# Performance work log

Hardware: AMD Instinct MI355X
Metric: run time of the kernel (lower is better)

Reference implementation:

```python
import jax, jax.numpy as jnp
import numpy as np

DIM = 64
B_GRAPHS = 16
N_NODES = 4096
N_EDGES = 16384
SLOPE = 0.01  # PyTorch leaky_relu default negative slope


def lrelu(x):
    return jnp.where(x >= 0, x, SLOPE * x)


def setup_inputs() -> dict:
    key = jax.random.key(0)
    ks = jax.random.split(key, 16)
    d = DIM

    def rn(k, shape, scale=0.05):
        return jax.random.normal(k, shape, dtype=jnp.float32) * scale

    def z(*s):
        return jnp.zeros(s, jnp.float32)

    return {
        "x": jax.random.normal(ks[0], (N_NODES, 3), dtype=jnp.float32),
        "edge_attr": jax.random.normal(ks[1], (N_EDGES, 4), dtype=jnp.float32),
        "edge_index": jax.random.randint(ks[2], (2, N_EDGES), 0, N_NODES),
        "batch": jnp.sort(jax.random.randint(ks[3], (N_NODES,), 0, B_GRAPHS)),
        # lin0
        "W0": rn(ks[4], (3, d)), "b0": z(d),
        # edge MLP: Linear(4,d) -> LeakyReLU -> Linear(d, d*d)
        "We1": rn(ks[5], (4, d)), "be1": z(d),
        "We2": rn(ks[6], (d, d * d), 0.01), "be2": z(d * d),
        # NNConv root weight + bias
        "root": rn(ks[7], (d, d)), "conv_b": z(d),
        # GRU(d, d)  (PyTorch layout: [3d, in] / [3d, hid], gate order r,z,n)
        "Wih": rn(ks[8], (3 * d, d)), "Whh": rn(ks[9], (3 * d, d)),
        "bih": z(3 * d), "bhh": z(3 * d),
        # Set2Set LSTM(2d, d)  (gate order i,f,g,o)
        "lWih": rn(ks[10], (4 * d, 2 * d)), "lWhh": rn(ks[11], (4 * d, d)),
        "lbih": z(4 * d), "lbhh": z(4 * d),
        # lin_out: Linear(2d, 2)
        "Wout": rn(ks[12], (2 * d, 2)), "bout": z(2),
    }


def _forward(x, edge_attr, W0, b0, We1, be1, We2, be2, root, conv_b,
             Wih, Whh, bih, bhh, lWih, lWhh, lbih, lbhh, Wout, bout,
             edge_index, batch):
    d = DIM
    N = x.shape[0]
    E = edge_attr.shape[0]
    src, dst = edge_index[0], edge_index[1]  # messages flow src(j) -> dst(i)

    out = lrelu(x @ W0 + b0)  # [N, d]
    h = out                    # GRU hidden state (h = out.unsqueeze(0))

    # Edge-conditioned weights: constant across the 6 iterations, compute once.
    he = lrelu(edge_attr @ We1 + be1)          # [E, d]
    W_e = (he @ We2 + be2).reshape(E, d, d)    # [E, d, d]
    deg = jax.ops.segment_sum(jnp.ones((E,), jnp.float32), dst, num_segments=N)
    inv_deg = (1.0 / jnp.maximum(deg, 1.0))[:, None]  # mean aggr, clamp like PyG

    for _ in range(6):
        # NNConv: gather x_j, per-edge matmul, scatter-mean, plus root term
        msg = jnp.einsum('ed,edf->ef', out[src], W_e)            # [E, d]
        agg = jax.ops.segment_sum(msg, dst, num_segments=N) * inv_deg
        m = lrelu(agg + out @ root + conv_b)                     # [N, d]
        # GRU cell (single step, PyTorch gate order r, z, n)
        gi = m @ Wih.T + bih
        gh = h @ Whh.T + bhh
        i_r, i_z, i_n = jnp.split(gi, 3, axis=-1)
        h_r, h_z, h_n = jnp.split(gh, 3, axis=-1)
        r = jax.nn.sigmoid(i_r + h_r)
        zg = jax.nn.sigmoid(i_z + h_z)
        n = jnp.tanh(i_n + r * h_n)
        h = (1.0 - zg) * n + zg * h
        out = h

    # Set2Set pooling, processing_steps = 1
    Bg = B_GRAPHS
    q_star = jnp.zeros((Bg, 2 * d), jnp.float32)
    hl = jnp.zeros((Bg, d), jnp.float32)
    cl = jnp.zeros((Bg, d), jnp.float32)
    gates = q_star @ lWih.T + lbih + hl @ lWhh.T + lbhh
    gi_, gf_, gg_, go_ = jnp.split(gates, 4, axis=-1)
    cl = jax.nn.sigmoid(gf_) * cl + jax.nn.sigmoid(gi_) * jnp.tanh(gg_)
    q = jax.nn.sigmoid(go_) * jnp.tanh(cl)         # [Bg, d]
    e = jnp.sum(out * q[batch], axis=-1)           # [N]
    emax = jax.ops.segment_max(e, batch, num_segments=Bg)
    a = jnp.exp(e - emax[batch])
    asum = jax.ops.segment_sum(a, batch, num_segments=Bg)
    a = a / asum[batch]                            # per-graph softmax attention
    rpool = jax.ops.segment_sum(a[:, None] * out, batch, num_segments=Bg)
    q_star = jnp.concatenate([q, rpool], axis=-1)  # [Bg, 2d]

    return q_star @ Wout + bout                    # [Bg, 2]


def reference(x, edge_attr, edge_index, batch, W0, b0, We1, be1, We2, be2,
              root, conv_b, Wih, Whh, bih, bhh, lWih, lWhh, lbih, lbhh,
              Wout, bout):
    return _forward(x, edge_attr, W0, b0, We1, be1, We2, be2, root, conv_b,
                    Wih, Whh, bih, bhh, lWih, lWhh, lbih, lbhh, Wout, bout,
                    edge_index, batch)
```

## Files before the change

kernel.cpp:

```cpp
#include <hip/hip_runtime.h>
#include <cstddef>

#define NE 16384
#define NN 4096
#define BG 16
#define CSTR 4416

__device__ __forceinline__ float lrelu(float v){ return v >= 0.f ? v : 0.01f*v; }
__device__ __forceinline__ float sigm(float v){ return 1.f/(1.f + expf(-v)); }

__global__ __launch_bounds__(256) void setup_kernel(
    const float* __restrict__ x, const float* __restrict__ ea,
    const int* __restrict__ ei,
    const float* __restrict__ W0, const float* __restrict__ b0,
    const float* __restrict__ We1, const float* __restrict__ be1,
    const float* __restrict__ We2, const float* __restrict__ be2,
    const float* __restrict__ root, const float* __restrict__ Whh,
    const float* __restrict__ Wih,
    float* __restrict__ Baug, float* __restrict__ WihT,
    float* __restrict__ h, float* __restrict__ he,
    int* __restrict__ deg, int* __restrict__ cnt)
{
    int t = blockIdx.x*256 + threadIdx.x;
    {
        int e = t >> 6, f = t & 63;
        float v = be1[f];
        #pragma unroll
        for (int d = 0; d < 4; ++d) v += ea[e*4+d]*We1[d*64+f];
        he[t] = lrelu(v);
    }
    if (t < 64*CSTR) {
        int d = t / CSTR, c = t - d*CSTR;
        float v;
        if (c < 4096)      v = We2[(c>>6)*4096 + d*64 + (c&63)];
        else if (c < 4160) v = be2[d*64 + (c-4096)];
        else if (c < 4352) v = Whh[(c-4160)*64 + d];
        else               v = root[d*64 + (c-4352)];
        Baug[t] = v;
    }
    if (t < NN*64) {
        int n = t >> 6, f = t & 63;
        float v = b0[f];
        #pragma unroll
        for (int d = 0; d < 3; ++d) v += x[n*3+d]*W0[d*64+f];
        h[t] = lrelu(v);
    }
    if (t < 12288) { int k = t / 192; WihT[t] = Wih[(t - k*192)*64 + k]; }
    if (t < NE) {
        atomicAdd(&deg[ei[NE + t]], 1);
        atomicAdd(&cnt[ei[t]], 1);
    }
}

__global__ __launch_bounds__(256) void scan_kernel(const int* __restrict__ cnt,
                                                   int* __restrict__ offs)
{
    __shared__ int ps[256];
    int t = threadIdx.x;
    int base = t*16;
    int loc[16];
    int s = 0;
    #pragma unroll
    for (int i = 0; i < 16; ++i) { loc[i] = s; s += cnt[base+i]; }
    ps[t] = s; __syncthreads();
    for (int off = 1; off < 256; off <<= 1) {
        int v = 0;
        if (t >= off) v = ps[t-off];
        __syncthreads();
        if (t >= off) ps[t] += v;
        __syncthreads();
    }
    int pre = (t == 0) ? 0 : ps[t-1];
    #pragma unroll
    for (int i = 0; i < 16; ++i) offs[base+i] = pre + loc[i];
    if (t == 255) offs[NN] = pre + s;
}

__global__ __launch_bounds__(256) void scatter_kernel(
    const int* __restrict__ ei, const int* __restrict__ offs,
    int* __restrict__ cnt,
    int* __restrict__ srcs, int* __restrict__ dsts, int* __restrict__ perm)
{
    int e = blockIdx.x*256 + threadIdx.x;
    if (e >= NE) return;
    int s = ei[e], d = ei[NE + e];
    int old = atomicSub(&cnt[s], 1);
    int pos = offs[s] + old - 1;
    srcs[pos] = s; dsts[pos] = d; perm[pos] = e;
}

__global__ __launch_bounds__(256) void inv_range_kernel(
    const int* __restrict__ deg, const int* __restrict__ batch,
    float* __restrict__ inv_deg, int* __restrict__ gstart, int* __restrict__ gend)
{
    int n = blockIdx.x*256 + threadIdx.x;
    if (n >= NN) return;
    inv_deg[n] = 1.f / fmaxf((float)deg[n], 1.f);
    int b  = batch[n];
    int bp = (n == 0)    ? -1 : batch[n-1];
    int bn = (n == NN-1) ? BG : batch[n+1];
    for (int g = bp+1; g <= b; ++g) gstart[g] = n;
    for (int g = b;   g <  bn; ++g) gend[g]   = n+1;
    if (n == 0)    for (int g = 0;   g < b;  ++g) gend[g]   = 0;
    if (n == NN-1) for (int g = b+1; g < BG; ++g) gstart[g] = NN;
}

__global__ __launch_bounds__(256) void gemm_big(
    const float* __restrict__ h, const float* __restrict__ Baug,
    float* __restrict__ C, float* __restrict__ agg)
{
    __shared__ float As[64][132];
    int t = threadIdx.x;
    int bx = blockIdx.x;
    int by = blockIdx.y;
    int m0 = by*128, c0 = bx*128;

    if (bx == 0) {
        float* a = agg + by*8192;
        #pragma unroll
        for (int i = 0; i < 32; ++i) a[t + i*256] = 0.f;
    }
    #pragma unroll
    for (int i = 0; i < 8; ++i) {
        int idx4 = t + i*256;
        int r = idx4 >> 4;
        int kc = (idx4 & 15) * 4;
        const float4 v = *(const float4*)(h + (size_t)(m0 + r)*64 + kc);
        As[kc+0][r] = v.x; As[kc+1][r] = v.y; As[kc+2][r] = v.z; As[kc+3][r] = v.w;
    }
    __syncthreads();

    int tx = t & 15, ty = t >> 4;
    int c_lo = c0 + tx*4, c_hi = c0 + 64 + tx*4;
    bool hi_ok = (c0 + 64) < CSTR;

    float acc[8][8];
    #pragma unroll
    for (int i = 0; i < 8; ++i)
        #pragma unroll
        for (int j = 0; j < 8; ++j) acc[i][j] = 0.f;

    #pragma unroll 8
    for (int k = 0; k < 64; ++k) {
        float4 a0 = *(const float4*)&As[k][ty*4];
        float4 a1 = *(const float4*)&As[k][64 + ty*4];
        float4 b0 = *(const float4*)(Baug + (size_t)k*CSTR + c_lo);
        float4 b1 = hi_ok ? *(const float4*)(Baug + (size_t)k*CSTR + c_hi)
                          : make_float4(0.f,0.f,0.f,0.f);
        float av[8] = {a0.x,a0.y,a0.z,a0.w,a1.x,a1.y,a1.z,a1.w};
        float bv[8] = {b0.x,b0.y,b0.z,b0.w,b1.x,b1.y,b1.z,b1.w};
        #pragma unroll
        for (int i = 0; i < 8; ++i)
            #pragma unroll
            for (int j = 0; j < 8; ++j) acc[i][j] += av[i]*bv[j];
    }

    #pragma unroll
    for (int i = 0; i < 8; ++i) {
        int m = m0 + (i>>2)*64 + ty*4 + (i&3);
        float* Cr = C + (size_t)m*CSTR;
        *(float4*)(Cr + c_lo) = make_float4(acc[i][0],acc[i][1],acc[i][2],acc[i][3]);
        if (hi_ok)
            *(float4*)(Cr + c_hi) = make_float4(acc[i][4],acc[i][5],acc[i][6],acc[i][7]);
    }
}

__global__ __launch_bounds__(256) void edge_kernel(
    const float* __restrict__ C, const float* __restrict__ he,
    const int* __restrict__ srcs, const int* __restrict__ dsts,
    const int* __restrict__ perm, float* __restrict__ agg)
{
    __shared__ float hs[256];
    int t = threadIdx.x;
    int e0 = blockIdx.x*4;
    int w = t >> 6, f = t & 63;
    int es = e0 + w;
    int pe = perm[es];
    hs[t] = he[(size_t)pe*64 + f];
    int src = srcs[es], dst = dsts[es];
    __syncthreads();
    const float* Cs = C + (size_t)src*CSTR;
    float m = Cs[4096 + f];
    #pragma unroll 8
    for (int k = 0; k < 64; ++k) m += hs[w*64+k] * Cs[k*64 + f];
    atomicAdd(&agg[(size_t)dst*64 + f], m);
}

__global__ __launch_bounds__(256) void node_kernel(
    const float* __restrict__ C, const float* __restrict__ agg,
    const float* __restrict__ inv_deg, const float* __restrict__ conv_b,
    const float* __restrict__ WihT, const float* __restrict__ bih,
    const float* __restrict__ bhh, float* __restrict__ h)
{
    __shared__ float WT[64][196];
    __shared__ float mT[64][18];
    int t = threadIdx.x;
    int n0 = blockIdx.x * 16;
    #pragma unroll
    for (int i = 0; i < 48; ++i) {
        int idx = t + i*256;
        int k = idx / 192;
        WT[k][idx - k*192] = WihT[idx];
    }
    #pragma unroll
    for (int i = 0; i < 4; ++i) {
        int idx = t + i*256;
        int n = idx >> 6, d = idx & 63;
        int gn = n0 + n;
        float v = agg[(size_t)gn*64 + d]*inv_deg[gn]
                + C[(size_t)gn*CSTR + 4352 + d] + conv_b[d];
        mT[d][n] = lrelu(v);
    }
    __syncthreads();

    int tx = t & 31, ty = t >> 5;
    float acc[2][2][3] = {};
    for (int k = 0; k < 64; ++k) {
        float2 a  = *(float2*)&mT[k][ty*2];
        float2 br = *(float2*)&WT[k][tx*2];
        float2 bz = *(float2*)&WT[k][64 + tx*2];
        float2 bn = *(float2*)&WT[k][128 + tx*2];
        acc[0][0][0] += a.x*br.x; acc[0][1][0] += a.x*br.y;
        acc[1][0][0] += a.y*br.x; acc[1][1][0] += a.y*br.y;
        acc[0][0][1] += a.x*bz.x; acc[0][1][1] += a.x*bz.y;
        acc[1][0][1] += a.y*bz.x; acc[1][1][1] += a.y*bz.y;
        acc[0][0][2] += a.x*bn.x; acc[0][1][2] += a.x*bn.y;
        acc[1][0][2] += a.y*bn.x; acc[1][1][2] += a.y*bn.y;
    }
    #pragma unroll
    for (int i = 0; i < 2; ++i) {
        int n = n0 + ty*2 + i;
        const float* Cn = C + (size_t)n*CSTR;
        #pragma unroll
        for (int j = 0; j < 2; ++j) {
            int g = tx*2 + j;
            float ir  = acc[i][j][0] + bih[g];
            float iz  = acc[i][j][1] + bih[64+g];
            float in_ = acc[i][j][2] + bih[128+g];
            float r  = sigm(ir  + Cn[4160 + g]       + bhh[g]);
            float z  = sigm(iz  + Cn[4160 + 64 + g]  + bhh[64+g]);
            float nn = tanhf(in_ + r*(Cn[4160 + 128 + g] + bhh[128+g]));
            float ho = h[(size_t)n*64 + g];
            h[(size_t)n*64 + g] = (1.f - z)*nn + z*ho;
        }
    }
}

__device__ __forceinline__ float q_val(const float* lbih, const float* lbhh, int g)
{
    float gi = lbih[g]     + lbhh[g];
    float gg = lbih[128+g] + lbhh[128+g];
    float go = lbih[192+g] + lbhh[192+g];
    return sigm(go)*tanhf(sigm(gi)*tanhf(gg));
}

__global__ __launch_bounds__(256) void e_kernel(
    const float* __restrict__ h, const float* __restrict__ lbih,
    const float* __restrict__ lbhh, float* __restrict__ e)
{
    __shared__ float qs[64];
    int t = threadIdx.x;
    if (t < 64) qs[t] = q_val(lbih, lbhh, t);
    __syncthreads();
    int w = t >> 6, f = t & 63;
    int n = blockIdx.x*4 + w;
    float p = h[(size_t)n*64 + f]*qs[f];
    #pragma unroll
    for (int off = 32; off; off >>= 1) p += __shfl_xor(p, off);
    if (f == 0) e[n] = p;
}

__global__ __launch_bounds__(1024) void pool_kernel(
    const float* __restrict__ h, float* __restrict__ e,
    const int* __restrict__ gstart, const int* __restrict__ gend,
    const float* __restrict__ lbih, const float* __restrict__ lbhh,
    const float* __restrict__ Wout, const float* __restrict__ bout,
    float* __restrict__ out)
{
    __shared__ float red[1024];
    __shared__ float rp[64];
    __shared__ float sval;
    int g = blockIdx.x, t = threadIdx.x;
    int s = gstart[g], en = gend[g];

    float mx = -1e30f;
    for (int n = s+t; n < en; n += 1024) mx = fmaxf(mx, e[n]);
    red[t] = mx; __syncthreads();
    for (int st = 512; st; st >>= 1) { if (t < st) red[t] = fmaxf(red[t], red[t+st]); __syncthreads(); }
    if (t == 0) sval = red[0];
    __syncthreads();
    float lmx = sval;
    __syncthreads();

    float sm = 0.f;
    for (int n = s+t; n < en; n += 1024) { float a = expf(e[n]-lmx); e[n] = a; sm += a; }
    red[t] = sm; __syncthreads();
    for (int st = 512; st; st >>= 1) { if (t < st) red[t] += red[t+st]; __syncthreads(); }
    if (t == 0) sval = (red[0] > 0.f) ? 1.f/red[0] : 0.f;
    __syncthreads();
    float inv_asum = sval;
    __syncthreads();

    int w = t >> 6, f = t & 63;
    float racc = 0.f;
    for (int n = s+w; n < en; n += 16) racc += e[n]*h[(size_t)n*64 + f];
    red[t] = racc; __syncthreads();
    if (w == 0) {
        float a = 0.f;
        #pragma unroll
        for (int i = 0; i < 16; ++i) a += red[i*64 + f];
        rp[f] = a*inv_asum;
    }
    __syncthreads();

    if (t < 64) {
        float qv = q_val(lbih, lbhh, t);
        float p0 = qv*Wout[t*2]   + rp[t]*Wout[(64+t)*2];
        float p1 = qv*Wout[t*2+1] + rp[t]*Wout[(64+t)*2+1];
        #pragma unroll
        for (int off = 32; off; off >>= 1) { p0 += __shfl_xor(p0, off); p1 += __shfl_xor(p1, off); }
        if (t == 0) { out[g*2] = p0 + bout[0]; out[g*2+1] = p1 + bout[1]; }
    }
}

extern "C" void kernel_launch(void* const* d_in, const int* in_sizes, int n_in,
                              void* d_out, int out_size, void* d_ws, size_t ws_size,
                              hipStream_t stream)
{
    const float* x      = (const float*)d_in[0];
    const float* ea     = (const float*)d_in[1];
    const int*   ei     = (const int*)  d_in[2];
    const int*   batch  = (const int*)  d_in[3];
    const float* W0     = (const float*)d_in[4];
    const float* b0     = (const float*)d_in[5];
    const float* We1    = (const float*)d_in[6];
    const float* be1    = (const float*)d_in[7];
    const float* We2    = (const float*)d_in[8];
    const float* be2    = (const float*)d_in[9];
    const float* root   = (const float*)d_in[10];
    const float* conv_b = (const float*)d_in[11];
    const float* Wih    = (const float*)d_in[12];
    const float* Whh    = (const float*)d_in[13];
    const float* bih    = (const float*)d_in[14];
    const float* bhh    = (const float*)d_in[15];
    const float* lbih   = (const float*)d_in[18];
    const float* lbhh   = (const float*)d_in[19];
    const float* Wout   = (const float*)d_in[20];
    const float* bout   = (const float*)d_in[21];
    float* out = (float*)d_out;

    float* W = (float*)d_ws;
    size_t off = 0;
    float* C       = W + off; off += (size_t)NN*CSTR;
    float* Baug    = W + off; off += (size_t)64*CSTR;
    float* h       = W + off; off += (size_t)NN*64;
    float* he      = W + off; off += (size_t)NE*64;
    float* agg     = W + off; off += (size_t)NN*64;
    float* WihT    = W + off; off += 12288;
    float* inv_deg = W + off; off += NN;
    float* e       = W + off; off += NN;
    int*   deg     = (int*)(W + off); off += NN;
    int*   cnt     = (int*)(W + off); off += NN;
    int*   offs    = (int*)(W + off); off += NN+1;
    int*   srcs    = (int*)(W + off); off += NE;
    int*   dsts    = (int*)(W + off); off += NE;
    int*   perm    = (int*)(W + off); off += NE;
    int*   gstart  = (int*)(W + off); off += BG;
    int*   gend    = (int*)(W + off); off += BG;

    hipMemsetAsync(deg, 0, 2*NN*sizeof(int), stream);
    setup_kernel<<<4096, 256, 0, stream>>>(x, ea, ei, W0, b0, We1, be1, We2, be2,
                                           root, Whh, Wih, Baug, WihT, h, he, deg, cnt);
    scan_kernel<<<1, 256, 0, stream>>>(cnt, offs);
    scatter_kernel<<<64, 256, 0, stream>>>(ei, offs, cnt, srcs, dsts, perm);
    inv_range_kernel<<<16, 256, 0, stream>>>(deg, batch, inv_deg, gstart, gend);

    for (int it = 0; it < 6; ++it) {
        gemm_big<<<dim3(35, 32), 256, 0, stream>>>(h, Baug, C, agg);
        edge_kernel<<<NE/4, 256, 0, stream>>>(C, he, srcs, dsts, perm, agg);
        node_kernel<<<NN/16, 256, 0, stream>>>(C, agg, inv_deg, conv_b, WihT, bih, bhh, h);
    }

    e_kernel<<<NN/4, 256, 0, stream>>>(h, lbih, lbhh, e);
    pool_kernel<<<BG, 1024, 0, stream>>>(h, e, gstart, gend, lbih, lbhh, Wout, bout, out);
}
```

Measured before the change: 658.3 us.

## Fuse per-node weight GEMM with edge messages in one conv kernel, drop C buffer

```diff
diff --git a/kernel.cpp b/kernel.cpp
--- a/kernel.cpp
+++ b/kernel.cpp
@@ -4,7 +4,8 @@
 #define NE 16384
 #define NN 4096
 #define BG 16
-#define CSTR 4416
+#define NT 16
+#define ACH 16
 
 __device__ __forceinline__ float lrelu(float v){ return v >= 0.f ? v : 0.01f*v; }
 __device__ __forceinline__ float sigm(float v){ return 1.f/(1.f + expf(-v)); }
@@ -14,10 +15,8 @@
     const int* __restrict__ ei,
     const float* __restrict__ W0, const float* __restrict__ b0,
     const float* __restrict__ We1, const float* __restrict__ be1,
-    const float* __restrict__ We2, const float* __restrict__ be2,
-    const float* __restrict__ root, const float* __restrict__ Whh,
-    const float* __restrict__ Wih,
-    float* __restrict__ Baug, float* __restrict__ WihT,
+    const float* __restrict__ Wih, const float* __restrict__ Whh,
+    float* __restrict__ WihT, float* __restrict__ WhhT,
     float* __restrict__ h, float* __restrict__ he,
     int* __restrict__ deg, int* __restrict__ cnt)
 {
@@ -29,15 +28,6 @@
         for (int d = 0; d < 4; ++d) v += ea[e*4+d]*We1[d*64+f];
         he[t] = lrelu(v);
     }
-    if (t < 64*CSTR) {
-        int d = t / CSTR, c = t - d*CSTR;
-        float v;
-        if (c < 4096)      v = We2[(c>>6)*4096 + d*64 + (c&63)];
-        else if (c < 4160) v = be2[d*64 + (c-4096)];
-        else if (c < 4352) v = Whh[(c-4160)*64 + d];
-        else               v = root[d*64 + (c-4352)];
-        Baug[t] = v;
-    }
     if (t < NN*64) {
         int n = t >> 6, f = t & 63;
         float v = b0[f];
@@ -45,7 +35,11 @@
         for (int d = 0; d < 3; ++d) v += x[n*3+d]*W0[d*64+f];
         h[t] = lrelu(v);
     }
-    if (t < 12288) { int k = t / 192; WihT[t] = Wih[(t - k*192)*64 + k]; }
+    if (t < 12288) {
+        int k = t / 192, g = t - k*192;
+        WihT[t] = Wih[g*64 + k];
+        WhhT[t] = Whh[g*64 + k];
+    }
     if (t < NE) {
         atomicAdd(&deg[ei[NE + t]], 1);
         atomicAdd(&cnt[ei[t]], 1);
@@ -87,6 +81,14 @@
     int old = atomicSub(&cnt[s], 1);
     int pos = offs[s] + old - 1;
     srcs[pos] = s; dsts[pos] = d; perm[pos] = e;
+}
+
+__global__ __launch_bounds__(256) void reorder_kernel(
+    const float* __restrict__ he, const int* __restrict__ perm,
+    float* __restrict__ he_srt)
+{
+    int t = blockIdx.x*256 + threadIdx.x;
+    he_srt[t] = he[(size_t)perm[t>>6]*64 + (t & 63)];
 }
 
 __global__ __launch_bounds__(256) void inv_range_kernel(
@@ -105,143 +107,185 @@
     if (n == NN-1) for (int g = b+1; g < BG; ++g) gstart[g] = NN;
 }
 
-__global__ __launch_bounds__(256) void gemm_big(
-    const float* __restrict__ h, const float* __restrict__ Baug,
-    float* __restrict__ C, float* __restrict__ agg)
-{
-    __shared__ float As[64][132];
-    int t = threadIdx.x;
-    int bx = blockIdx.x;
-    int by = blockIdx.y;
-    int m0 = by*128, c0 = bx*128;
-
-    if (bx == 0) {
-        float* a = agg + by*8192;
-        #pragma unroll
-        for (int i = 0; i < 32; ++i) a[t + i*256] = 0.f;
-    }
-    #pragma unroll
-    for (int i = 0; i < 8; ++i) {
-        int idx4 = t + i*256;
-        int r = idx4 >> 4;
-        int kc = (idx4 & 15) * 4;
-        const float4 v = *(const float4*)(h + (size_t)(m0 + r)*64 + kc);
-        As[kc+0][r] = v.x; As[kc+1][r] = v.y; As[kc+2][r] = v.z; As[kc+3][r] = v.w;
-    }
-    __syncthreads();
-
-    int tx = t & 15, ty = t >> 4;
-    int c_lo = c0 + tx*4, c_hi = c0 + 64 + tx*4;
-    bool hi_ok = (c0 + 64) < CSTR;
-
-    float acc[8][8];
-    #pragma unroll
-    for (int i = 0; i < 8; ++i)
-        #pragma unroll
-        for (int j = 0; j < 8; ++j) acc[i][j] = 0.f;
-
+__global__ __launch_bounds__(1024) void conv_kernel(
+    const float* __restrict__ h, const float* __restrict__ We2,
+    const float* __restrict__ be2, const float* __restrict__ he_srt,
+    const int* __restrict__ offs, const int* __restrict__ srcs,
+    const int* __restrict__ dsts, float* __restrict__ agg)
+{
+    __shared__ float hsT[64][NT];
+    __shared__ float Tb [NT][64];
+    __shared__ float Tc [ACH][NT][64];
+    int t  = threadIdx.x;
+    int n0 = blockIdx.x * NT;
+
+    {
+        int n = t >> 6, i = t & 63;
+        hsT[i][n] = h[(size_t)(n0+n)*64 + i];
+    }
+    __syncthreads();
+    {
+        int n = t >> 6, f = t & 63;
+        float acc = 0.f;
+        #pragma unroll 8
+        for (int i = 0; i < 64; ++i) acc += hsT[i][n] * be2[i*64+f];
+        Tb[n][f] = acc;
+    }
+
+    int ebase = offs[n0];
+    int ecnt  = offs[n0+NT] - ebase;
+    int eend  = ebase + ecnt;
+    int slot  = t >> 4;
+    int f4    = (t & 15) * 4;
+    int e0 = ebase + slot, e1 = ebase + slot + 64;
+    int nl0 = -1, dt0 = 0, nl1 = -1, dt1 = 0;
+    if (slot < ecnt)       { nl0 = srcs[e0] - n0; dt0 = dsts[e0]; }
+    if (slot + 64 < ecnt)  { nl1 = srcs[e1] - n0; dt1 = dsts[e1]; }
+    float4 m0 = {0,0,0,0}, m1 = {0,0,0,0};
+
+    int aT = t >> 6;
+    int fT = (t & 15) * 4;
+    int nT = ((t >> 4) & 3) * 4;
+
+    for (int c = 0; c < 4; ++c) {
+        const float* Wp = We2 + ((size_t)(c*ACH + aT))*4096 + fT;
+        float4 A0 = {0,0,0,0}, A1 = {0,0,0,0}, A2 = {0,0,0,0}, A3 = {0,0,0,0};
+        #pragma unroll 8
+        for (int i = 0; i < 64; ++i) {
+            float4 w  = *(const float4*)(Wp + (size_t)i*64);
+            float4 hv = *(const float4*)&hsT[i][nT];
+            A0.x += hv.x*w.x; A0.y += hv.x*w.y; A0.z += hv.x*w.z; A0.w += hv.x*w.w;
+            A1.x += hv.y*w.x; A1.y += hv.y*w.y; A1.z += hv.y*w.z; A1.w += hv.y*w.w;
+            A2.x += hv.z*w.x; A2.y += hv.z*w.y; A2.z += hv.z*w.z; A2.w += hv.z*w.w;
+            A3.x += hv.w*w.x; A3.y += hv.w*w.y; A3.z += hv.w*w.z; A3.w += hv.w*w.w;
+        }
+        __syncthreads();
+        *(float4*)&Tc[aT][nT+0][fT] = A0;
+        *(float4*)&Tc[aT][nT+1][fT] = A1;
+        *(float4*)&Tc[aT][nT+2][fT] = A2;
+        *(float4*)&Tc[aT][nT+3][fT] = A3;
+        __syncthreads();
+
+        if (nl0 >= 0) {
+            const float* hep = he_srt + (size_t)e0*64 + c*ACH;
+            #pragma unroll
+            for (int a = 0; a < ACH; ++a) {
+                float hv = hep[a];
+                float4 tv = *(const float4*)&Tc[a][nl0][f4];
+                m0.x += hv*tv.x; m0.y += hv*tv.y; m0.z += hv*tv.z; m0.w += hv*tv.w;
+            }
+        }
+        if (nl1 >= 0) {
+            const float* hep = he_srt + (size_t)e1*64 + c*ACH;
+            #pragma unroll
+            for (int a = 0; a < ACH; ++a) {
+                float hv = hep[a];
+                float4 tv = *(const float4*)&Tc[a][nl1][f4];
+                m1.x += hv*tv.x; m1.y += hv*tv.y; m1.z += hv*tv.z; m1.w += hv*tv.w;
+            }
+        }
+        for (int e = ebase + 128 + slot; e < eend; e += 64) {
+            int nl = srcs[e] - n0, dt = dsts[e];
+            const float* hep = he_srt + (size_t)e*64 + c*ACH;
+            float4 pm = {0,0,0,0};
+            #pragma unroll
+            for (int a = 0; a < ACH; ++a) {
+                float hv = hep[a];
+                float4 tv = *(const float4*)&Tc[a][nl][f4];
+                pm.x += hv*tv.x; pm.y += hv*tv.y; pm.z += hv*tv.z; pm.w += hv*tv.w;
+            }
+            if (c == 0) {
+                float4 b = *(const float4*)&Tb[nl][f4];
+                pm.x += b.x; pm.y += b.y; pm.z += b.z; pm.w += b.w;
+            }
+            float* ap = agg + (size_t)dt*64 + f4;
+            atomicAdd(ap+0, pm.x); atomicAdd(ap+1, pm.y);
+            atomicAdd(ap+2, pm.z); atomicAdd(ap+3, pm.w);
+        }
+    }
+
+    if (nl0 >= 0) {
+        float4 b = *(const float4*)&Tb[nl0][f4];
+        float* ap = agg + (size_t)dt0*64 + f4;
+        atomicAdd(ap+0, m0.x+b.x); atomicAdd(ap+1, m0.y+b.y);
+        atomicAdd(ap+2, m0.z+b.z); atomicAdd(ap+3, m0.w+b.w);
+    }
+    if (nl1 >= 0) {
+        float4 b = *(const float4*)&Tb[nl1][f4];
+        float* ap = agg + (size_t)dt1*64 + f4;
+        atomicAdd(ap+0, m1.x+b.x); atomicAdd(ap+1, m1.y+b.y);
+        atomicAdd(ap+2, m1.z+b.z); atomicAdd(ap+3, m1.w+b.w);
+    }
+}
+
+__global__ __launch_bounds__(512) void node_kernel(
+    const float* __restrict__ WihT, const float* __restrict__ WhhT,
+    const float* __restrict__ root, const float* __restrict__ conv_b,
+    const float* __restrict__ inv_deg, const float* __restrict__ bih,
+    const float* __restrict__ bhh, float* __restrict__ h,
+    float* __restrict__ agg)
+{
+    __shared__ float WT[64][392];
+    __shared__ float hT[64][34];
+    __shared__ float mT[64][34];
+    int t  = threadIdx.x;
+    int n0 = blockIdx.x * 32;
+
+    #pragma unroll
+    for (int i = 0; i < 24; ++i) {
+        int idx = t + i*512;
+        int k = idx / 192, c = idx - k*192;
+        WT[k][c]       = WihT[idx];
+        WT[k][196 + c] = WhhT[idx];
+    }
+    #pragma unroll
+    for (int i = 0; i < 4; ++i) {
+        int idx = t + i*512;
+        int n = idx >> 6, d = idx & 63;
+        hT[d][n] = h[(size_t)(n0+n)*64 + d];
+    }
+    __syncthreads();
+    #pragma unroll
+    for (int i = 0; i < 4; ++i) {
+        int idx = t + i*512;
+        int n = idx >> 6, d = idx & 63;
+        int gn = n0 + n;
+        float v = agg[(size_t)gn*64 + d]*inv_deg[gn] + conv_b[d];
+        agg[(size_t)gn*64 + d] = 0.f;
+        #pragma unroll 8
+        for (int k = 0; k < 64; ++k) v += hT[k][n]*root[k*64 + d];
+        mT[d][n] = lrelu(v);
+    }
+    __syncthreads();
+
+    int tx = t & 31, ty = t >> 5;
+    float ai[2][2][3] = {{{0.f}}};
+    float ah[2][2][3] = {{{0.f}}};
     #pragma unroll 8
     for (int k = 0; k < 64; ++k) {
-        float4 a0 = *(const float4*)&As[k][ty*4];
-        float4 a1 = *(const float4*)&As[k][64 + ty*4];
-        float4 b0 = *(const float4*)(Baug + (size_t)k*CSTR + c_lo);
-        float4 b1 = hi_ok ? *(const float4*)(Baug + (size_t)k*CSTR + c_hi)
-                          : make_float4(0.f,0.f,0.f,0.f);
-        float av[8] = {a0.x,a0.y,a0.z,a0.w,a1.x,a1.y,a1.z,a1.w};
-        float bv[8] = {b0.x,b0.y,b0.z,b0.w,b1.x,b1.y,b1.z,b1.w};
-        #pragma unroll
-        for (int i = 0; i < 8; ++i)
-            #pragma unroll
-            for (int j = 0; j < 8; ++j) acc[i][j] += av[i]*bv[j];
-    }
-
-    #pragma unroll
-    for (int i = 0; i < 8; ++i) {
-        int m = m0 + (i>>2)*64 + ty*4 + (i&3);
-        float* Cr = C + (size_t)m*CSTR;
-        *(float4*)(Cr + c_lo) = make_float4(acc[i][0],acc[i][1],acc[i][2],acc[i][3]);
-        if (hi_ok)
-            *(float4*)(Cr + c_hi) = make_float4(acc[i][4],acc[i][5],acc[i][6],acc[i][7]);
-    }
-}
-
-__global__ __launch_bounds__(256) void edge_kernel(
-    const float* __restrict__ C, const float* __restrict__ he,
-    const int* __restrict__ srcs, const int* __restrict__ dsts,
-    const int* __restrict__ perm, float* __restrict__ agg)
-{
-    __shared__ float hs[256];
-    int t = threadIdx.x;
-    int e0 = blockIdx.x*4;
-    int w = t >> 6, f = t & 63;
-    int es = e0 + w;
-    int pe = perm[es];
-    hs[t] = he[(size_t)pe*64 + f];
-    int src = srcs[es], dst = dsts[es];
-    __syncthreads();
-    const float* Cs = C + (size_t)src*CSTR;
-    float m = Cs[4096 + f];
-    #pragma unroll 8
-    for (int k = 0; k < 64; ++k) m += hs[w*64+k] * Cs[k*64 + f];
-    atomicAdd(&agg[(size_t)dst*64 + f], m);
-}
-
-__global__ __launch_bounds__(256) void node_kernel(
-    const float* __restrict__ C, const float* __restrict__ agg,
-    const float* __restrict__ inv_deg, const float* __restrict__ conv_b,
-    const float* __restrict__ WihT, const float* __restrict__ bih,
-    const float* __restrict__ bhh, float* __restrict__ h)
-{
-    __shared__ float WT[64][196];
-    __shared__ float mT[64][18];
-    int t = threadIdx.x;
-    int n0 = blockIdx.x * 16;
-    #pragma unroll
-    for (int i = 0; i < 48; ++i) {
-        int idx = t + i*256;
-        int k = idx / 192;
-        WT[k][idx - k*192] = WihT[idx];
-    }
-    #pragma unroll
-    for (int i = 0; i < 4; ++i) {
-        int idx = t + i*256;
-        int n = idx >> 6, d = idx & 63;
-        int gn = n0 + n;
-        float v = agg[(size_t)gn*64 + d]*inv_deg[gn]
-                + C[(size_t)gn*CSTR + 4352 + d] + conv_b[d];
-        mT[d][n] = lrelu(v);
-    }
-    __syncthreads();
-
-    int tx = t & 31, ty = t >> 5;
-    float acc[2][2][3] = {};
-    for (int k = 0; k < 64; ++k) {
-        float2 a  = *(float2*)&mT[k][ty*2];
-        float2 br = *(float2*)&WT[k][tx*2];
-        float2 bz = *(float2*)&WT[k][64 + tx*2];
-        float2 bn = *(float2*)&WT[k][128 + tx*2];
-        acc[0][0][0] += a.x*br.x; acc[0][1][0] += a.x*br.y;
-        acc[1][0][0] += a.y*br.x; acc[1][1][0] += a.y*br.y;
-        acc[0][0][1] += a.x*bz.x; acc[0][1][1] += a.x*bz.y;
-        acc[1][0][1] += a.y*bz.x; acc[1][1][1] += a.y*bz.y;
-        acc[0][0][2] += a.x*bn.x; acc[0][1][2] += a.x*bn.y;
-        acc[1][0][2] += a.y*bn.x; acc[1][1][2] += a.y*bn.y;
+        float2 am = *(float2*)&mT[k][ty*2];
+        float2 av = *(float2*)&hT[k][ty*2];
+        #pragma unroll
+        for (int g = 0; g < 3; ++g) {
+            float2 bi = *(float2*)&WT[k][g*64 + tx*2];
+            float2 bh = *(float2*)&WT[k][196 + g*64 + tx*2];
+            ai[0][0][g] += am.x*bi.x; ai[0][1][g] += am.x*bi.y;
+            ai[1][0][g] += am.y*bi.x; ai[1][1][g] += am.y*bi.y;
+            ah[0][0][g] += av.x*bh.x; ah[0][1][g] += av.x*bh.y;
+            ah[1][0][g] += av.y*bh.x; ah[1][1][g] += av.y*bh.y;
+        }
     }
     #pragma unroll
     for (int i = 0; i < 2; ++i) {
-        int n = n0 + ty*2 + i;
-        const float* Cn = C + (size_t)n*CSTR;
+        int n = ty*2 + i, gn = n0 + n;
         #pragma unroll
         for (int j = 0; j < 2; ++j) {
             int g = tx*2 + j;
-            float ir  = acc[i][j][0] + bih[g];
-            float iz  = acc[i][j][1] + bih[64+g];
-            float in_ = acc[i][j][2] + bih[128+g];
-            float r  = sigm(ir  + Cn[4160 + g]       + bhh[g]);
-            float z  = sigm(iz  + Cn[4160 + 64 + g]  + bhh[64+g]);
-            float nn = tanhf(in_ + r*(Cn[4160 + 128 + g] + bhh[128+g]));
-            float ho = h[(size_t)n*64 + g];
-            h[(size_t)n*64 + g] = (1.f - z)*nn + z*ho;
+            float r  = sigm(ai[i][j][0] + bih[g]      + ah[i][j][0] + bhh[g]);
+            float z  = sigm(ai[i][j][1] + bih[64+g]   + ah[i][j][1] + bhh[64+g]);
+            float nn = tanhf(ai[i][j][2] + bih[128+g] + r*(ah[i][j][2] + bhh[128+g]));
+            float ho = hT[g][n];
+            h[(size_t)gn*64 + g] = (1.f - z)*nn + z*ho;
         }
     }
 }
@@ -351,12 +395,12 @@
 
     float* W = (float*)d_ws;
     size_t off = 0;
-    float* C       = W + off; off += (size_t)NN*CSTR;
-    float* Baug    = W + off; off += (size_t)64*CSTR;
     float* h       = W + off; off += (size_t)NN*64;
     float* he      = W + off; off += (size_t)NE*64;
+    float* he_srt  = W + off; off += (size_t)NE*64;
     float* agg     = W + off; off += (size_t)NN*64;
     float* WihT    = W + off; off += 12288;
+    float* WhhT    = W + off; off += 12288;
     float* inv_deg = W + off; off += NN;
     float* e       = W + off; off += NN;
     int*   deg     = (int*)(W + off); off += NN;
@@ -369,16 +413,19 @@
     int*   gend    = (int*)(W + off); off += BG;
 
     hipMemsetAsync(deg, 0, 2*NN*sizeof(int), stream);
-    setup_kernel<<<4096, 256, 0, stream>>>(x, ea, ei, W0, b0, We1, be1, We2, be2,
-                                           root, Whh, Wih, Baug, WihT, h, he, deg, cnt);
+    hipMemsetAsync(agg, 0, (size_t)NN*64*sizeof(float), stream);
+    setup_kernel<<<4096, 256, 0, stream>>>(x, ea, ei, W0, b0, We1, be1, Wih, Whh,
+                                           WihT, WhhT, h, he, deg, cnt);
     scan_kernel<<<1, 256, 0, stream>>>(cnt, offs);
     scatter_kernel<<<64, 256, 0, stream>>>(ei, offs, cnt, srcs, dsts, perm);
+    reorder_kernel<<<4096, 256, 0, stream>>>(he, perm, he_srt);
     inv_range_kernel<<<16, 256, 0, stream>>>(deg, batch, inv_deg, gstart, gend);
 
     for (int it = 0; it < 6; ++it) {
-        gemm_big<<<dim3(35, 32), 256, 0, stream>>>(h, Baug, C, agg);
-        edge_kernel<<<NE/4, 256, 0, stream>>>(C, he, srcs, dsts, perm, agg);
-        node_kernel<<<NN/16, 256, 0, stream>>>(C, agg, inv_deg, conv_b, WihT, bih, bhh, h);
+        conv_kernel<<<NN/NT, 1024, 0, stream>>>(h, We2, be2, he_srt,
+                                                offs, srcs, dsts, agg);
+        node_kernel<<<NN/32, 512, 0, stream>>>(WihT, WhhT, root, conv_b,
+                                               inv_deg, bih, bhh, h, agg);
     }
 
     e_kernel<<<NN/4, 256, 0, stream>>>(h, lbih, lbhh, e);
```

New measurement: 573.1 us. -12.9%, faster.
